# Kernel tuning notes

Hardware: AMD Instinct MI355X
Metric: run time of the kernel (lower is better)

## Reference

```python
import jax, jax.numpy as jnp
import numpy as np
from jax import lax


def _conv1d(x, w, b, stride, pad):
    # x: [N, 1, L], w: [1, 1, K]
    y = lax.conv_general_dilated(x, w, (stride,), [(pad, pad)],
                                 dimension_numbers=('NCH', 'OIH', 'NCH'))
    return y + b[None, :, None]


def _maxpool1d(x, k, stride, pad):
    # torch MaxPool1d semantics: pad with -inf, window max
    return lax.reduce_window(x, -jnp.inf, lax.max,
                             (1, 1, k), (1, 1, stride),
                             ((0, 0), (0, 0), (pad, pad)))


def setup_inputs() -> dict:
    key = jax.random.key(0)
    ks = jax.random.split(key, 14)
    bs, n, T = 64, 1024, 1200
    return {
        'input':   jax.random.normal(ks[0], (bs, n, T), jnp.float32),
        'conv1_w': jax.random.normal(ks[1], (1, 1, 10), jnp.float32) * 0.3,
        'conv1_b': jax.random.normal(ks[2], (1,), jnp.float32) * 0.1,
        'conv2_w': jax.random.normal(ks[3], (1, 1, 3), jnp.float32) * 0.5,
        'conv2_b': jax.random.normal(ks[4], (1,), jnp.float32) * 0.1,
        'conv3_w': jax.random.normal(ks[5], (1, 1, 4), jnp.float32) * 0.5,
        'conv3_b': jax.random.normal(ks[6], (1,), jnp.float32) * 0.1,
        'gcn1_w':  jax.random.normal(ks[7], (30, 30), jnp.float32) * 0.18,
        'gcn1_b':  jax.random.normal(ks[8], (30,), jnp.float32) * 0.1,
        'gcn2_w':  jax.random.normal(ks[9], (4, 4), jnp.float32) * 0.5,
        'gcn2_b':  jax.random.normal(ks[10], (4,), jnp.float32) * 0.1,
        'cls_w':   jax.random.normal(ks[11], (3, n), jnp.float32) * 0.03,
        'cls_b':   jax.random.normal(ks[12], (3,), jnp.float32) * 0.1,
    }


def reference(input, conv1_w, conv1_b, conv2_w, conv2_b, conv3_w, conv3_b,
              gcn1_w, gcn1_b, gcn2_w, gcn2_b, cls_w, cls_b):
    bs, n, T = input.shape
    # Per-node 1-channel conv chain: fold nodes into the batch dim (replaces
    # the original Python loop over num_nodes issuing tiny Conv1d launches).
    x = input.reshape(bs * n, 1, T)
    h = jax.nn.relu(_conv1d(x, conv1_w, conv1_b, 8, 1))   # L: 1200 -> 150
    h = jax.nn.relu(_maxpool1d(h, 5, 5, 0))               # 150 -> 30
    # NOTE: original applies gcn1 to t_layer_out[2] here, but overwrites an
    # already-consumed list entry -> output is DEAD w.r.t. the final result.
    # (GCNConv over the all-ones adjacency == mean over nodes @ W.T + b.)
    h = jax.nn.relu(_conv1d(h, conv2_w, conv2_b, 3, 0))   # 30 -> 10
    h = jax.nn.relu(_maxpool1d(h, 3, 3, 1))               # 10 -> 4
    # Same dead-code situation for gcn2 on t_layer_out[4].
    h = jax.nn.relu(_conv1d(h, conv3_w, conv3_b, 1, 0))   # 4 -> 1
    feat = h.reshape(bs, n)                               # L5 == 1
    logits = feat @ cls_w.T + cls_b
    return jax.nn.softmax(logits, axis=1)
```

## Files before the change

kernel.cpp:

```cpp
#include <hip/hip_runtime.h>


#define NROWS 65536
#define ROWS_PER_BLOCK 4
#define STRIDE_F 1220
#define STRIDE_F4 305
#define NBLOCKS (NROWS / ROWS_PER_BLOCK)

__global__ __launch_bounds__(128, 4) void fused_chain_kernel(
    const float* __restrict__ input,
    const float* __restrict__ w1g, const float* __restrict__ b1g,
    const float* __restrict__ w2g, const float* __restrict__ b2g,
    const float* __restrict__ w3g, const float* __restrict__ b3g,
    float* __restrict__ feat)
{
    __shared__ __align__(16) float xs[ROWS_PER_BLOCK * STRIDE_F];

    const int tid = threadIdx.x;
    const int blk = blockIdx.x;

    const float4* src = (const float4*)(input + (size_t)blk * 4800);
    #pragma unroll
    for (int it = 0; it < 10; ++it) {
        const int i = tid + it * 128;
        if (i < 1200) {
            const float4 vv = src[i];
            const int r = i / 300;
            const int c4 = i - r * 300;
            ((float4*)xs)[r * STRIDE_F4 + c4] = vv;
        }
    }

    float w1[10];
    #pragma unroll
    for (int k = 0; k < 10; ++k) w1[k] = w1g[k];
    const float b1 = b1g[0];

    __syncthreads();

    const int lane = tid & 63;
    const int wave = tid >> 6;
    const int half = lane >> 5;
    const int w = lane & 31;
    const int rib = wave * 2 + half;

    const float* xr = xs + rib * STRIDE_F + w * 40;
    float pmax = 0.0f;
    if (w < 30) {
        float v[42];
        v[0] = (w == 0) ? 0.0f : xr[-1];
        #pragma unroll
        for (int m = 1; m <= 40; ++m) v[m] = xr[m - 1];
        v[41] = (w == 29) ? 0.0f : xr[40];

        #pragma unroll
        for (int i = 0; i < 5; ++i) {
            float acc = b1;
            #pragma unroll
            for (int k = 0; k < 10; ++k) acc = fmaf(w1[k], v[8 * i + k], acc);
            pmax = fmaxf(pmax, acc);
        }
    }

    const int base = lane & 32;
    const int jj = (w < 10) ? w : 9;
    const float pa = __shfl(pmax, base + 3 * jj, 64);
    const float pb = __shfl(pmax, base + 3 * jj + 1, 64);
    const float pc = __shfl(pmax, base + 3 * jj + 2, 64);
    const float w2a = w2g[0], w2b = w2g[1], w2c = w2g[2];
    const float y2 = fmaxf(fmaf(w2c, pc, fmaf(w2b, pb, fmaf(w2a, pa, b2g[0]))), 0.0f);

    const float t1 = __shfl(y2, base + 1, 64);
    const float t2 = __shfl(y2, base + 2, 64);
    const float t3 = __shfl(y2, base + 3, 64);
    const float t4 = __shfl(y2, base + 4, 64);
    const float t5 = __shfl(y2, base + 5, 64);
    const float t6 = __shfl(y2, base + 6, 64);
    const float t7 = __shfl(y2, base + 7, 64);
    const float t8 = __shfl(y2, base + 8, 64);
    const float t9 = __shfl(y2, base + 9, 64);
    if (w == 0) {
        const float q0 = fmaxf(y2, t1);
        const float q1 = fmaxf(fmaxf(t2, t3), t4);
        const float q2 = fmaxf(fmaxf(t5, t6), t7);
        const float q3 = fmaxf(t8, t9);
        float f = b3g[0];
        f = fmaf(w3g[0], q0, f);
        f = fmaf(w3g[1], q1, f);
        f = fmaf(w3g[2], q2, f);
        f = fmaf(w3g[3], q3, f);
        feat[(size_t)blk * ROWS_PER_BLOCK + rib] = fmaxf(f, 0.0f);
    }
}

__global__ __launch_bounds__(256) void classifier_kernel(
    const float* __restrict__ feat,
    const float* __restrict__ cls_w,
    const float* __restrict__ cls_b,
    float* __restrict__ out)
{
    const int b = blockIdx.x;
    const int tid = threadIdx.x;

    float s0 = 0.0f, s1 = 0.0f, s2 = 0.0f;
    for (int n = tid; n < 1024; n += 256) {
        const float f = feat[b * 1024 + n];
        s0 = fmaf(f, cls_w[n], s0);
        s1 = fmaf(f, cls_w[1024 + n], s1);
        s2 = fmaf(f, cls_w[2048 + n], s2);
    }
    #pragma unroll
    for (int off = 32; off > 0; off >>= 1) {
        s0 += __shfl_down(s0, off, 64);
        s1 += __shfl_down(s1, off, 64);
        s2 += __shfl_down(s2, off, 64);
    }
    __shared__ float red[3][4];
    const int wave = tid >> 6;
    if ((tid & 63) == 0) {
        red[0][wave] = s0;
        red[1][wave] = s1;
        red[2][wave] = s2;
    }
    __syncthreads();
    if (tid == 0) {
        const float l0 = red[0][0] + red[0][1] + red[0][2] + red[0][3] + cls_b[0];
        const float l1 = red[1][0] + red[1][1] + red[1][2] + red[1][3] + cls_b[1];
        const float l2 = red[2][0] + red[2][1] + red[2][2] + red[2][3] + cls_b[2];
        const float m = fmaxf(l0, fmaxf(l1, l2));
        const float e0 = expf(l0 - m);
        const float e1 = expf(l1 - m);
        const float e2 = expf(l2 - m);
        const float inv = 1.0f / (e0 + e1 + e2);
        out[b * 3 + 0] = e0 * inv;
        out[b * 3 + 1] = e1 * inv;
        out[b * 3 + 2] = e2 * inv;
    }
}

extern "C" void kernel_launch(void* const* d_in, const int* in_sizes, int n_in,
                              void* d_out, int out_size, void* d_ws, size_t ws_size,
                              hipStream_t stream) {
    const float* input   = (const float*)d_in[0];
    const float* conv1_w = (const float*)d_in[1];
    const float* conv1_b = (const float*)d_in[2];
    const float* conv2_w = (const float*)d_in[3];
    const float* conv2_b = (const float*)d_in[4];
    const float* conv3_w = (const float*)d_in[5];
    const float* conv3_b = (const float*)d_in[6];
    const float* cls_w   = (const float*)d_in[11];
    const float* cls_b   = (const float*)d_in[12];

    float* featbuf = (float*)d_ws;
    float* out     = (float*)d_out;

    fused_chain_kernel<<<NBLOCKS, 128, 0, stream>>>(
        input, conv1_w, conv1_b, conv2_w, conv2_b, conv3_w, conv3_b, featbuf);
    classifier_kernel<<<64, 256, 0, stream>>>(featbuf, cls_w, cls_b, out);
}
```

Measured before the change: 433.8 us.

## Make fused chain kernel persistent with register-prefetched row generations

After: 516.9 us. 19.2% more time.

```diff
diff --git a/kernel.cpp b/kernel.cpp
--- a/kernel.cpp
+++ b/kernel.cpp
@@ -2,94 +2,117 @@
 
 
 #define NROWS 65536
-#define ROWS_PER_BLOCK 4
+#define ROWS_PER_GEN 4
+#define GENS 8
+#define NBLOCKS 2048
 #define STRIDE_F 1220
 #define STRIDE_F4 305
-#define NBLOCKS (NROWS / ROWS_PER_BLOCK)
+#define GEN_F4 1200
 
-__global__ __launch_bounds__(128, 4) void fused_chain_kernel(
+__global__ __launch_bounds__(256, 4) void fused_chain_kernel(
     const float* __restrict__ input,
     const float* __restrict__ w1g, const float* __restrict__ b1g,
     const float* __restrict__ w2g, const float* __restrict__ b2g,
     const float* __restrict__ w3g, const float* __restrict__ b3g,
     float* __restrict__ feat)
 {
-    __shared__ __align__(16) float xs[ROWS_PER_BLOCK * STRIDE_F];
+    __shared__ __align__(16) float xs[ROWS_PER_GEN * STRIDE_F];
 
     const int tid = threadIdx.x;
     const int blk = blockIdx.x;
-
-    const float4* src = (const float4*)(input + (size_t)blk * 4800);
-    #pragma unroll
-    for (int it = 0; it < 10; ++it) {
-        const int i = tid + it * 128;
-        if (i < 1200) {
-            const float4 vv = src[i];
-            const int r = i / 300;
-            const int c4 = i - r * 300;
-            ((float4*)xs)[r * STRIDE_F4 + c4] = vv;
-        }
-    }
+    const float4* src = (const float4*)(input + (size_t)blk * 32 * 1200);
 
     float w1[10];
     #pragma unroll
     for (int k = 0; k < 10; ++k) w1[k] = w1g[k];
     const float b1 = b1g[0];
+    const float w2a = w2g[0], w2b = w2g[1], w2c = w2g[2], b2 = b2g[0];
+    const float w3a = w3g[0], w3b = w3g[1], w3c = w3g[2], w3d = w3g[3];
+    const float b3 = b3g[0];
 
-    __syncthreads();
+    const int wv = tid >> 6;
+    const int w  = tid & 63;
 
-    const int lane = tid & 63;
-    const int wave = tid >> 6;
-    const int half = lane >> 5;
-    const int w = lane & 31;
-    const int rib = wave * 2 + half;
-
-    const float* xr = xs + rib * STRIDE_F + w * 40;
-    float pmax = 0.0f;
-    if (w < 30) {
-        float v[42];
-        v[0] = (w == 0) ? 0.0f : xr[-1];
-        #pragma unroll
-        for (int m = 1; m <= 40; ++m) v[m] = xr[m - 1];
-        v[41] = (w == 29) ? 0.0f : xr[40];
-
-        #pragma unroll
-        for (int i = 0; i < 5; ++i) {
-            float acc = b1;
-            #pragma unroll
-            for (int k = 0; k < 10; ++k) acc = fmaf(w1[k], v[8 * i + k], acc);
-            pmax = fmaxf(pmax, acc);
-        }
+    float4 pf[5];
+    #pragma unroll
+    for (int it = 0; it < 5; ++it) {
+        const int i = tid + it * 256;
+        if (i < GEN_F4) pf[it] = src[i];
     }
 
-    const int base = lane & 32;
-    const int jj = (w < 10) ? w : 9;
-    const float pa = __shfl(pmax, base + 3 * jj, 64);
-    const float pb = __shfl(pmax, base + 3 * jj + 1, 64);
-    const float pc = __shfl(pmax, base + 3 * jj + 2, 64);
-    const float w2a = w2g[0], w2b = w2g[1], w2c = w2g[2];
-    const float y2 = fmaxf(fmaf(w2c, pc, fmaf(w2b, pb, fmaf(w2a, pa, b2g[0]))), 0.0f);
+    #pragma unroll 1
+    for (int g = 0; g < GENS; ++g) {
+        #pragma unroll
+        for (int it = 0; it < 5; ++it) {
+            const int i = tid + it * 256;
+            if (i < GEN_F4) {
+                const int r = i / 300;
+                const int c4 = i - r * 300;
+                ((float4*)xs)[r * STRIDE_F4 + c4] = pf[it];
+            }
+        }
+        __syncthreads();
 
-    const float t1 = __shfl(y2, base + 1, 64);
-    const float t2 = __shfl(y2, base + 2, 64);
-    const float t3 = __shfl(y2, base + 3, 64);
-    const float t4 = __shfl(y2, base + 4, 64);
-    const float t5 = __shfl(y2, base + 5, 64);
-    const float t6 = __shfl(y2, base + 6, 64);
-    const float t7 = __shfl(y2, base + 7, 64);
-    const float t8 = __shfl(y2, base + 8, 64);
-    const float t9 = __shfl(y2, base + 9, 64);
-    if (w == 0) {
-        const float q0 = fmaxf(y2, t1);
-        const float q1 = fmaxf(fmaxf(t2, t3), t4);
-        const float q2 = fmaxf(fmaxf(t5, t6), t7);
-        const float q3 = fmaxf(t8, t9);
-        float f = b3g[0];
-        f = fmaf(w3g[0], q0, f);
-        f = fmaf(w3g[1], q1, f);
-        f = fmaf(w3g[2], q2, f);
-        f = fmaf(w3g[3], q3, f);
-        feat[(size_t)blk * ROWS_PER_BLOCK + rib] = fmaxf(f, 0.0f);
+        if (g + 1 < GENS) {
+            const float4* nsrc = src + (size_t)(g + 1) * GEN_F4;
+            #pragma unroll
+            for (int it = 0; it < 5; ++it) {
+                const int i = tid + it * 256;
+                if (i < GEN_F4) pf[it] = nsrc[i];
+            }
+        }
+
+        float pmax = 0.0f;
+        if (w < 30) {
+            const float* xr = xs + wv * STRIDE_F + w * 40;
+            float v[42];
+            v[0] = (w == 0) ? 0.0f : xr[-1];
+            const float4* xr4 = (const float4*)xr;
+            #pragma unroll
+            for (int q = 0; q < 10; ++q) {
+                const float4 t = xr4[q];
+                v[1 + 4 * q] = t.x; v[2 + 4 * q] = t.y;
+                v[3 + 4 * q] = t.z; v[4 + 4 * q] = t.w;
+            }
+            v[41] = (w == 29) ? 0.0f : xr[40];
+
+            #pragma unroll
+            for (int i = 0; i < 5; ++i) {
+                float acc = b1;
+                #pragma unroll
+                for (int k = 0; k < 10; ++k) acc = fmaf(w1[k], v[8 * i + k], acc);
+                pmax = fmaxf(pmax, acc);
+            }
+        }
+
+        const int jj = (w < 10) ? w : 9;
+        const float pa = __shfl(pmax, 3 * jj, 64);
+        const float pb = __shfl(pmax, 3 * jj + 1, 64);
+        const float pc = __shfl(pmax, 3 * jj + 2, 64);
+        const float y2 = fmaxf(fmaf(w2c, pc, fmaf(w2b, pb, fmaf(w2a, pa, b2))), 0.0f);
+
+        const float t1 = __shfl(y2, 1, 64);
+        const float t2 = __shfl(y2, 2, 64);
+        const float t3 = __shfl(y2, 3, 64);
+        const float t4 = __shfl(y2, 4, 64);
+        const float t5 = __shfl(y2, 5, 64);
+        const float t6 = __shfl(y2, 6, 64);
+        const float t7 = __shfl(y2, 7, 64);
+        const float t8 = __shfl(y2, 8, 64);
+        const float t9 = __shfl(y2, 9, 64);
+        if (w == 0) {
+            const float q0 = fmaxf(y2, t1);
+            const float q1 = fmaxf(fmaxf(t2, t3), t4);
+            const float q2 = fmaxf(fmaxf(t5, t6), t7);
+            const float q3 = fmaxf(t8, t9);
+            float f = b3;
+            f = fmaf(w3a, q0, f);
+            f = fmaf(w3b, q1, f);
+            f = fmaf(w3c, q2, f);
+            f = fmaf(w3d, q3, f);
+            feat[blk * 32 + g * ROWS_PER_GEN + wv] = fmaxf(f, 0.0f);
+        }
+        __syncthreads();
     }
 }
 
@@ -154,7 +177,7 @@
     float* featbuf = (float*)d_ws;
     float* out     = (float*)d_out;
 
-    fused_chain_kernel<<<NBLOCKS, 128, 0, stream>>>(
+    fused_chain_kernel<<<NBLOCKS, 256, 0, stream>>>(
         input, conv1_w, conv1_b, conv2_w, conv2_b, conv3_w, conv3_b, featbuf);
     classifier_kernel<<<64, 256, 0, stream>>>(featbuf, cls_w, cls_b, out);
 }
```
